# Kernel tuning notes

Measured on AMD Instinct MI355X. Metric: run time of the kernel, lower is better.

The kernel has to match this reference:

```python
import jax, jax.numpy as jnp
import numpy as np

N = 32768        # num_nodes
D = 256          # hidden_dim
H = 8            # num_heads
DH = D // H      # head_dim
S = 4            # num_scales
CS = max(3, N // 10)          # cluster size (pos=None path)
C = (N + CS - 1) // CS        # num_clusters
EPS = 1e-5


def setup_inputs() -> dict:
    key = jax.random.key(0)
    ks = jax.random.split(key, 16)
    w = 0.02
    return {
        "x": jax.random.normal(ks[0], (N, D), dtype=jnp.float32),
        "edge_index": jax.random.randint(ks[1], (2, 16 * N), 0, N),
        "batch": jnp.zeros((N,), dtype=jnp.int32),
        # per-scale AttentionPooling params (stacked over S)
        "Wk": jax.random.normal(ks[2], (S, D, D), dtype=jnp.float32) * w,
        "bk": jnp.zeros((S, D), dtype=jnp.float32),
        "Wv": jax.random.normal(ks[3], (S, D, D), dtype=jnp.float32) * w,
        "bv": jnp.zeros((S, D), dtype=jnp.float32),
        "Wo": jax.random.normal(ks[4], (S, D, D), dtype=jnp.float32) * w,
        "bo": jnp.zeros((S, D), dtype=jnp.float32),
        "pool_query": jax.random.normal(ks[5], (S, H, DH), dtype=jnp.float32),
        # scale fusion params
        "Wf1": jax.random.normal(ks[6], (S * D, D), dtype=jnp.float32) * w,
        "bf1": jnp.zeros((D,), dtype=jnp.float32),
        "ln_g": jnp.ones((D,), dtype=jnp.float32),
        "ln_b": jnp.zeros((D,), dtype=jnp.float32),
        "Wf2": jax.random.normal(ks[7], (D, D), dtype=jnp.float32) * w,
        "bf2": jnp.zeros((D,), dtype=jnp.float32),
    }


def reference(x, edge_index, batch, Wk, bk, Wv, bv, Wo, bo, pool_query,
              Wf1, bf1, ln_g, ln_b, Wf2, bf2):
    # clusters from pos=None branch: arange(N) // cluster_size (same at all scales)
    clusters = jnp.arange(N) // CS                                  # [N]
    scale = DH ** -0.5

    # all S scales vectorized (params stacked on axis s)
    keys = (jnp.einsum('nd,sde->nse', x, Wk) + bk).reshape(N, S, H, DH)
    values = (jnp.einsum('nd,sde->nse', x, Wv) + bv).reshape(N, S, H, DH)

    # pool_query is identical for every node -> scores[n,s,h] = <k, q> * scale
    scores = jnp.einsum('nshd,shd->nsh', keys, pool_query) * scale  # [N,S,H]

    # per-cluster softmax over the node dim (segment softmax)
    smax = jax.ops.segment_max(scores, clusters, num_segments=C)    # [C,S,H]
    ex = jnp.exp(scores - smax[clusters])
    denom = jax.ops.segment_sum(ex, clusters, num_segments=C)
    weights = ex / denom[clusters]                                  # [N,S,H]

    # attended values, scatter-mean over clusters
    attended = (weights[..., None] * values).reshape(N, S, D)       # [N,S,D]
    counts = jax.ops.segment_sum(jnp.ones((N,), dtype=x.dtype), clusters, num_segments=C)
    pooled = jax.ops.segment_sum(attended, clusters, num_segments=C) / counts[:, None, None]

    # out_proj then gather back to nodes
    out = jnp.einsum('csd,sde->cse', pooled, Wo) + bo               # [C,S,D]
    node = out[clusters]                                            # [N,S,D]

    # scale fusion: Linear -> LayerNorm -> GELU -> (Dropout eval=id) -> Linear
    combined = node.reshape(N, S * D)
    h = combined @ Wf1 + bf1
    mu = jnp.mean(h, axis=-1, keepdims=True)
    var = jnp.mean(jnp.square(h - mu), axis=-1, keepdims=True)
    h = (h - mu) / jnp.sqrt(var + EPS) * ln_g + ln_b
    h = jax.nn.gelu(h, approximate=False)
    fused = h @ Wf2 + bf2                                           # [N,D]
    return fused
```

## Files before the change

kernel.cpp:

```cpp
#include <hip/hip_runtime.h>
#include <math.h>


namespace {
constexpr int N   = 32768;
constexpr int CS  = 3276;
constexpr int CPN = 128;
constexpr int CPC = 26;
constexpr int NB  = CPC*10 + 1;

constexpr size_t CQ_OFF   = 0;
constexpr size_t WQBF_OFF = 32;
constexpr size_t PART_OFF = WQBF_OFF + 4096;
constexpr size_t PS_OFF   = PART_OFF + (size_t)NB*8192;
constexpr size_t XW_OFF   = PS_OFF + 352;
constexpr size_t PL_OFF   = XW_OFF + 90112;
constexpr size_t OL_OFF   = PL_OFF + 11264;
constexpr size_t HP_OFF   = OL_OFF + 11264;
constexpr size_t HL_OFF   = HP_OFF + 11264;
constexpr size_t FP_OFF   = HL_OFF + 2816;
}

typedef __attribute__((ext_vector_type(8))) short short8;
typedef __attribute__((ext_vector_type(4))) float f32x4;

__device__ __forceinline__ unsigned f2bf(float f){
  unsigned u = __float_as_uint(f);
  unsigned r = u + 0x7FFFu + ((u >> 16) & 1u);
  return r >> 16;
}

__global__ __launch_bounds__(256) void ka(const float* __restrict__ Wk, const float* __restrict__ bk,
                                          const float* __restrict__ pq, float* __restrict__ ws){
  int b = blockIdx.x, t = threadIdx.x;
  const float scale = 0.17677669529663688f;
  if (b < 32){
    __shared__ float row[256];
    int s = b >> 3, h = b & 7;
    const float* wrow = Wk + ((size_t)s<<16) + (size_t)t*256 + h*32;
    const float* q = pq + (s*8 + h)*32;
    float a = 0.f;
#pragma unroll
    for (int j=0;j<32;j++) a = fmaf(wrow[j], q[j], a);
    row[t] = a*scale;
    __syncthreads();
    if (t < 32){
      int ks = t & 7, kg2 = t >> 3;
      const float* src = row + ks*32 + kg2*8;
      uint4 p;
      p.x = f2bf(src[0]) | (f2bf(src[1]) << 16);
      p.y = f2bf(src[2]) | (f2bf(src[3]) << 16);
      p.z = f2bf(src[4]) | (f2bf(src[5]) << 16);
      p.w = f2bf(src[6]) | (f2bf(src[7]) << 16);
      int Nt = b >> 4, l15b = b & 15;
      ((uint4*)(ws + WQBF_OFF))[(size_t)(Nt*8 + ks)*64 + l15b + 16*kg2] = p;
    }
  } else {
    if (t < 32){
      int s = t >> 3, h = t & 7;
      const float* br = bk + s*256 + h*32;
      const float* q = pq + t*32;
      float a = 0.f;
#pragma unroll
      for (int j=0;j<32;j++) a = fmaf(br[j], q[j], a);
      ws[CQ_OFF + t] = a*scale;
    }
    for (int i = t; i < 352; i += 256) ws[PS_OFF + i] = 0.f;
  }
}

__global__ __launch_bounds__(512,6) void kbd7(const float* __restrict__ x, float* __restrict__ ws){
  int b = blockIdx.x, t = threadIdx.x;
  int c  = (b < 260) ? (b / CPC) : 10;
  int wi = (b < 260) ? (b % CPC) : 0;
  int n0 = c*CS + wi*CPN;
  int n1 = min(n0 + CPN, min((c+1)*CS, N));
  int cnt = n1 - n0;

  __shared__ unsigned short xtb[64*264];
  __shared__ float sw[64*36];
  __shared__ float psb[16*32];

  int wv = t >> 6, lane = t & 63;
  int Mt = wv & 3, Nt = wv >> 2;
  int l15 = lane & 15, kg = lane >> 4;
  int arow = Mt*16 + l15;
  uint4 bfr[8];
  const uint4* WQBF4 = (const uint4*)(ws + WQBF_OFF);
#pragma unroll
  for (int ks=0; ks<8; ++ks) bfr[ks] = WQBF4[(size_t)(Nt*8 + ks)*64 + lane];
  float cqv = ws[CQ_OFF + Nt*16 + l15];
  int shc = Nt*16 + l15;

  int shq = t >> 6, dq = t & 63;
  float acc[16];
#pragma unroll
  for (int q=0;q<16;q++) acc[q] = 0.f;
  float s4 = 0.f;

  const float4* X4 = (const float4*)x;
  int nst = (cnt + 63) >> 6;
  for (int st=0; st<nst; ++st){
    int base = n0 + st*64;
    int lim = min(64, cnt - st*64);
    if (st) __syncthreads();
#pragma unroll
    for (int k=0;k<8;k++){
      int f = t + k*512;
      int j = f >> 6, c4 = f & 63;
      if (base + j < N){
        float4 v = X4[(size_t)(base+j)*64 + c4];
        uint2 p;
        p.x = f2bf(v.x) | (f2bf(v.y) << 16);
        p.y = f2bf(v.z) | (f2bf(v.w) << 16);
        *(uint2*)(xtb + j*264 + c4*4) = p;
      }
    }
    __syncthreads();
    f32x4 acc1 = {0.f, 0.f, 0.f, 0.f};
#pragma unroll
    for (int ks=0; ks<8; ++ks){
      union { uint4 q; short8 v; } A, B;
      A.q = *(const uint4*)(xtb + arow*264 + ks*32 + kg*8);
      B.q = bfr[ks];
      acc1 = __builtin_amdgcn_mfma_f32_16x16x32_bf16(A.v, B.v, acc1, 0, 0, 0);
    }
#pragma unroll
    for (int r=0;r<4;r++){
      int jl = Mt*16 + kg*4 + r;
      float e = __expf(acc1[r] + cqv);
      sw[jl*36 + shc] = e;
      if (st*64 + jl < cnt) s4 += e;
    }
    __syncthreads();
#pragma unroll 4
    for (int j=0;j<lim;++j){
      uint2 u = *(const uint2*)(xtb + j*264 + dq*4);
      float x0 = __uint_as_float(u.x << 16);
      float x1 = __uint_as_float(u.x & 0xffff0000u);
      float x2 = __uint_as_float(u.y << 16);
      float x3 = __uint_as_float(u.y & 0xffff0000u);
      float4 wv2 = *(const float4*)(sw + j*36 + shq*4);
      acc[0]  = fmaf(wv2.x, x0, acc[0]);  acc[1]  = fmaf(wv2.x, x1, acc[1]);
      acc[2]  = fmaf(wv2.x, x2, acc[2]);  acc[3]  = fmaf(wv2.x, x3, acc[3]);
      acc[4]  = fmaf(wv2.y, x0, acc[4]);  acc[5]  = fmaf(wv2.y, x1, acc[5]);
      acc[6]  = fmaf(wv2.y, x2, acc[6]);  acc[7]  = fmaf(wv2.y, x3, acc[7]);
      acc[8]  = fmaf(wv2.z, x0, acc[8]);  acc[9]  = fmaf(wv2.z, x1, acc[9]);
      acc[10] = fmaf(wv2.z, x2, acc[10]); acc[11] = fmaf(wv2.z, x3, acc[11]);
      acc[12] = fmaf(wv2.w, x0, acc[12]); acc[13] = fmaf(wv2.w, x1, acc[13]);
      acc[14] = fmaf(wv2.w, x2, acc[14]); acc[15] = fmaf(wv2.w, x3, acc[15]);
    }
  }
  psb[(Mt*4 + kg)*32 + shc] = s4;
  __syncthreads();
  if (t < 32){
    float S = 0.f;
#pragma unroll
    for (int k=0;k<16;k++) S += psb[k*32 + t];
    unsafeAtomicAdd(ws + PS_OFF + (size_t)c*32 + t, S);
  }
  float* pr = ws + PART_OFF + (size_t)b*8192;
#pragma unroll
  for (int i=0;i<4;i++)
    *(float4*)(pr + (size_t)(shq*4+i)*256 + dq*4) =
      make_float4(acc[i*4], acc[i*4+1], acc[i*4+2], acc[i*4+3]);
}

__global__ __launch_bounds__(256) void ke2(float* __restrict__ ws){
  int b = blockIdx.x, t = threadIdx.x;
  int c = b >> 5, sh = b & 31;
  int nch = (c < 10) ? CPC : 1;
  int cb  = (c < 10) ? c*CPC : 260;
  float rden = 1.0f / ws[PS_OFF + (size_t)c*32 + sh];
  const float* part = ws + PART_OFF + (size_t)sh*256 + t;
  float a = 0.f;
  for (int k=0;k<nch;k++) a += part[(size_t)(cb+k)*8192];
  ws[XW_OFF + (size_t)c*8192 + (size_t)sh*256 + t] = a * rden;
}

__global__ __launch_bounds__(256) void kp(float* __restrict__ ws,
    const float* __restrict__ Wv, const float* __restrict__ bv){
  int b = blockIdx.x; int c = b >> 4, rem = b & 15, s = rem >> 2, eq = rem & 3;
  int t = threadIdx.x, e64 = t & 63, dq = t >> 6;
  int e = eq*64 + e64, h = e >> 5;
  const float* xr = ws + XW_OFF + (size_t)c*8192 + (size_t)(s*8 + h)*256 + dq*64;
  const float* wv = Wv + (size_t)s*65536 + (size_t)(dq*64)*256 + e;
  float a = 0.f;
#pragma unroll 8
  for (int d=0; d<64; ++d) a = fmaf(wv[(size_t)d*256], xr[d], a);
  __shared__ float red[4][64];
  red[dq][e64] = a;
  __syncthreads();
  if (t < 64){
    float rcnt = (c < 10) ? (1.0f/(float)CS) : 0.125f;
    float p = (red[0][t]+red[1][t]+red[2][t]+red[3][t] + bv[s*256 + eq*64 + t]) * rcnt;
    ws[PL_OFF + (size_t)c*1024 + s*256 + eq*64 + t] = p;
  }
}

__global__ __launch_bounds__(256) void ko(float* __restrict__ ws,
    const float* __restrict__ Wo, const float* __restrict__ bo){
  int b = blockIdx.x; int c = b >> 4, rem = b & 15, s = rem >> 2, eq = rem & 3;
  int t = threadIdx.x, e64 = t & 63, dq = t >> 6;
  int e = eq*64 + e64;
  const float* pr = ws + PL_OFF + (size_t)c*1024 + s*256 + dq*64;
  const float* wo = Wo + (size_t)s*65536 + (size_t)(dq*64)*256 + e;
  float a = 0.f;
#pragma unroll 8
  for (int d=0; d<64; ++d) a = fmaf(wo[(size_t)d*256], pr[d], a);
  __shared__ float red[4][64];
  red[dq][e64] = a;
  __syncthreads();
  if (t < 64)
    ws[OL_OFF + (size_t)c*1024 + s*256 + eq*64 + t] =
      red[0][t]+red[1][t]+red[2][t]+red[3][t] + bo[s*256 + eq*64 + t];
}

__global__ __launch_bounds__(256) void kf1(const float* __restrict__ Wf1, float* __restrict__ ws){
  int b = blockIdx.x; int c = b >> 4, fq = (b >> 2) & 3, kq = b & 3;
  int t = threadIdx.x, f64 = t & 63, ks = t >> 6;
  const float* ol = ws + OL_OFF + (size_t)c*1024 + kq*256 + ks*64;
  const float* wf = Wf1 + (size_t)(kq*256 + ks*64)*256 + fq*64 + f64;
  float a = 0.f;
#pragma unroll 8
  for (int i=0; i<64; ++i) a = fmaf(wf[(size_t)i*256], ol[i], a);
  __shared__ float red[4][64];
  red[ks][f64] = a;
  __syncthreads();
  if (t < 64)
    ws[HP_OFF + (size_t)(c*4 + kq)*256 + fq*64 + t] = red[0][t]+red[1][t]+red[2][t]+red[3][t];
}

__global__ __launch_bounds__(256) void kln(float* __restrict__ ws, const float* __restrict__ bf1,
    const float* __restrict__ lng, const float* __restrict__ lnb){
  int c = blockIdx.x, t = threadIdx.x;
  __shared__ float rs1[4], rs2[4];
  float hacc = bf1[t];
#pragma unroll
  for (int q=0;q<4;q++) hacc += ws[HP_OFF + (size_t)(c*4+q)*256 + t];
  float s1 = hacc, s2v = hacc*hacc;
  for (int off=32; off>0; off>>=1){ s1 += __shfl_down(s1, off, 64); s2v += __shfl_down(s2v, off, 64); }
  int wid = t>>6, lane = t&63;
  if (lane==0){ rs1[wid]=s1; rs2[wid]=s2v; }
  __syncthreads();
  float S1 = rs1[0]+rs1[1]+rs1[2]+rs1[3];
  float S2 = rs2[0]+rs2[1]+rs2[2]+rs2[3];
  float mu = S1*(1.0f/256.0f);
  float var = S2*(1.0f/256.0f) - mu*mu;
  float rsig = rsqrtf(var + 1e-5f);
  float hn = (hacc - mu)*rsig*lng[t] + lnb[t];
  float ge = 0.5f*hn*(1.0f + erff(hn*0.70710678118654752f));
  ws[HL_OFF + (size_t)c*256 + t] = ge;
}

__global__ __launch_bounds__(256) void kf2(const float* __restrict__ Wf2, float* __restrict__ ws){
  int b = blockIdx.x; int c = b >> 4, gq = (b >> 2) & 3, kq = b & 3;
  int t = threadIdx.x, g64 = t & 63, ks = t >> 6;
  const float* hp = ws + HL_OFF + (size_t)c*256 + kq*64 + ks*16;
  const float* wf = Wf2 + (size_t)(kq*64 + ks*16)*256 + gq*64 + g64;
  float a = 0.f;
#pragma unroll
  for (int i=0; i<16; ++i) a = fmaf(wf[(size_t)i*256], hp[i], a);
  __shared__ float red[4][64];
  red[ks][g64] = a;
  __syncthreads();
  if (t < 64)
    ws[FP_OFF + (size_t)(c*4 + kq)*256 + gq*64 + t] = red[0][t]+red[1][t]+red[2][t]+red[3][t];
}

__global__ __launch_bounds__(256) void kbc2(const float* __restrict__ ws, float4* __restrict__ out,
                                            const float* __restrict__ bf2){
  unsigned bidx = blockIdx.x, t = threadIdx.x;
  unsigned idx = bidx*256u + t;
  unsigned c = (bidx*4u) / (unsigned)CS;
  __shared__ float4 row[64];
  if (t < 64){
    const float4* FP4 = (const float4*)(ws + FP_OFF);
    float4 s0 = FP4[(c*4+0)*64 + t];
    float4 s1 = FP4[(c*4+1)*64 + t];
    float4 s2 = FP4[(c*4+2)*64 + t];
    float4 s3 = FP4[(c*4+3)*64 + t];
    float4 bb = ((const float4*)bf2)[t];
    row[t] = make_float4(s0.x+s1.x+s2.x+s3.x+bb.x, s0.y+s1.y+s2.y+s3.y+bb.y,
                         s0.z+s1.z+s2.z+s3.z+bb.z, s0.w+s1.w+s2.w+s3.w+bb.w);
  }
  __syncthreads();
  out[idx] = row[t & 63u];
}

extern "C" void kernel_launch(void* const* d_in, const int* in_sizes, int n_in,
                              void* d_out, int out_size, void* d_ws, size_t ws_size,
                              hipStream_t stream) {
  const float* x   = (const float*)d_in[0];
  const float* Wk  = (const float*)d_in[3];
  const float* bk  = (const float*)d_in[4];
  const float* Wv  = (const float*)d_in[5];
  const float* bv  = (const float*)d_in[6];
  const float* Wo  = (const float*)d_in[7];
  const float* bo  = (const float*)d_in[8];
  const float* pq  = (const float*)d_in[9];
  const float* Wf1 = (const float*)d_in[10];
  const float* bf1 = (const float*)d_in[11];
  const float* lng = (const float*)d_in[12];
  const float* lnb = (const float*)d_in[13];
  const float* Wf2 = (const float*)d_in[14];
  const float* bf2 = (const float*)d_in[15];
  float* ws = (float*)d_ws;
  float4* out = (float4*)d_out;

  hipLaunchKernelGGL(ka,   dim3(33),   dim3(256), 0, stream, Wk, bk, pq, ws);
  hipLaunchKernelGGL(kbd7, dim3(NB),   dim3(512), 0, stream, x, ws);
  hipLaunchKernelGGL(ke2,  dim3(352),  dim3(256), 0, stream, ws);
  hipLaunchKernelGGL(kp,   dim3(176),  dim3(256), 0, stream, ws, Wv, bv);
  hipLaunchKernelGGL(ko,   dim3(176),  dim3(256), 0, stream, ws, Wo, bo);
  hipLaunchKernelGGL(kf1,  dim3(176),  dim3(256), 0, stream, Wf1, ws);
  hipLaunchKernelGGL(kln,  dim3(11),   dim3(256), 0, stream, ws, bf1, lng, lnb);
  hipLaunchKernelGGL(kf2,  dim3(176),  dim3(256), 0, stream, Wf2, ws);
  hipLaunchKernelGGL(kbc2, dim3(8192), dim3(256), 0, stream, ws, out, bf2);
}
```

Before: 70.44 us.

## Drop LDS staging of x in pooling kernel, halve chunk size, fuse LayerNorm into Wf2

The pooling kernel no longer stages bf16-converted x tiles in shared memory. Each wave now loads its MFMA A-operand straight from global memory, and the weighted-value accumulation reads fp32 x directly from global memory. Each block now handles 64 nodes instead of 128, which doubles the block count to 521 and lowers the occupancy hint. The LayerNorm+GELU kernel is merged into the Wf2 matvec kernel, which recomputes the normalization per block and saves one launch. The pooled sum now uses full-precision x instead of bf16 x, and x is read twice from global memory/cache rather than once.

```diff
diff --git a/kernel.cpp b/kernel.cpp
--- a/kernel.cpp
+++ b/kernel.cpp
@@ -5,8 +5,7 @@
 namespace {
 constexpr int N   = 32768;
 constexpr int CS  = 3276;
-constexpr int CPN = 128;
-constexpr int CPC = 26;
+constexpr int CPC = 52;
 constexpr int NB  = CPC*10 + 1;
 
 constexpr size_t CQ_OFF   = 0;
@@ -17,8 +16,7 @@
 constexpr size_t PL_OFF   = XW_OFF + 90112;
 constexpr size_t OL_OFF   = PL_OFF + 11264;
 constexpr size_t HP_OFF   = OL_OFF + 11264;
-constexpr size_t HL_OFF   = HP_OFF + 11264;
-constexpr size_t FP_OFF   = HL_OFF + 2816;
+constexpr size_t FP_OFF   = HP_OFF + 11264;
 }
 
 typedef __attribute__((ext_vector_type(8))) short short8;
@@ -69,89 +67,49 @@
   }
 }
 
-__global__ __launch_bounds__(512,6) void kbd7(const float* __restrict__ x, float* __restrict__ ws){
+__global__ __launch_bounds__(512,4) void kbd8(const float* __restrict__ x, float* __restrict__ ws){
   int b = blockIdx.x, t = threadIdx.x;
-  int c  = (b < 260) ? (b / CPC) : 10;
-  int wi = (b < 260) ? (b % CPC) : 0;
-  int n0 = c*CS + wi*CPN;
-  int n1 = min(n0 + CPN, min((c+1)*CS, N));
+  int c  = (b < 520) ? (b / CPC) : 10;
+  int wi = (b < 520) ? (b % CPC) : 0;
+  int n0 = c*CS + wi*64;
+  int n1 = min(n0 + 64, min((c+1)*CS, N));
   int cnt = n1 - n0;
 
-  __shared__ unsigned short xtb[64*264];
   __shared__ float sw[64*36];
   __shared__ float psb[16*32];
 
   int wv = t >> 6, lane = t & 63;
-  int Mt = wv & 3, Nt = wv >> 2;
-  int l15 = lane & 15, kg = lane >> 4;
-  int arow = Mt*16 + l15;
-  uint4 bfr[8];
-  const uint4* WQBF4 = (const uint4*)(ws + WQBF_OFF);
-#pragma unroll
-  for (int ks=0; ks<8; ++ks) bfr[ks] = WQBF4[(size_t)(Nt*8 + ks)*64 + lane];
-  float cqv = ws[CQ_OFF + Nt*16 + l15];
-  int shc = Nt*16 + l15;
-
-  int shq = t >> 6, dq = t & 63;
-  float acc[16];
-#pragma unroll
-  for (int q=0;q<16;q++) acc[q] = 0.f;
-  float s4 = 0.f;
-
-  const float4* X4 = (const float4*)x;
-  int nst = (cnt + 63) >> 6;
-  for (int st=0; st<nst; ++st){
-    int base = n0 + st*64;
-    int lim = min(64, cnt - st*64);
-    if (st) __syncthreads();
-#pragma unroll
-    for (int k=0;k<8;k++){
-      int f = t + k*512;
-      int j = f >> 6, c4 = f & 63;
-      if (base + j < N){
-        float4 v = X4[(size_t)(base+j)*64 + c4];
-        uint2 p;
-        p.x = f2bf(v.x) | (f2bf(v.y) << 16);
-        p.y = f2bf(v.z) | (f2bf(v.w) << 16);
-        *(uint2*)(xtb + j*264 + c4*4) = p;
-      }
-    }
-    __syncthreads();
+  {
+    int Mt = wv & 3, Nt = wv >> 2;
+    int l15 = lane & 15, kg = lane >> 4;
+    int grow = min(n0 + Mt*16 + l15, N-1);
+    const float* xrow = x + (size_t)grow*256;
+    const uint4* WQBF4 = (const uint4*)(ws + WQBF_OFF);
+    float cqv = ws[CQ_OFF + Nt*16 + l15];
     f32x4 acc1 = {0.f, 0.f, 0.f, 0.f};
 #pragma unroll
     for (int ks=0; ks<8; ++ks){
+      float4 x0 = *(const float4*)(xrow + ks*32 + kg*8);
+      float4 x1 = *(const float4*)(xrow + ks*32 + kg*8 + 4);
       union { uint4 q; short8 v; } A, B;
-      A.q = *(const uint4*)(xtb + arow*264 + ks*32 + kg*8);
-      B.q = bfr[ks];
+      A.q.x = f2bf(x0.x) | (f2bf(x0.y) << 16);
+      A.q.y = f2bf(x0.z) | (f2bf(x0.w) << 16);
+      A.q.z = f2bf(x1.x) | (f2bf(x1.y) << 16);
+      A.q.w = f2bf(x1.z) | (f2bf(x1.w) << 16);
+      B.q = WQBF4[(size_t)(Nt*8 + ks)*64 + lane];
       acc1 = __builtin_amdgcn_mfma_f32_16x16x32_bf16(A.v, B.v, acc1, 0, 0, 0);
     }
+    int shc = Nt*16 + l15;
+    float s4 = 0.f;
 #pragma unroll
     for (int r=0;r<4;r++){
       int jl = Mt*16 + kg*4 + r;
       float e = __expf(acc1[r] + cqv);
       sw[jl*36 + shc] = e;
-      if (st*64 + jl < cnt) s4 += e;
-    }
-    __syncthreads();
-#pragma unroll 4
-    for (int j=0;j<lim;++j){
-      uint2 u = *(const uint2*)(xtb + j*264 + dq*4);
-      float x0 = __uint_as_float(u.x << 16);
-      float x1 = __uint_as_float(u.x & 0xffff0000u);
-      float x2 = __uint_as_float(u.y << 16);
-      float x3 = __uint_as_float(u.y & 0xffff0000u);
-      float4 wv2 = *(const float4*)(sw + j*36 + shq*4);
-      acc[0]  = fmaf(wv2.x, x0, acc[0]);  acc[1]  = fmaf(wv2.x, x1, acc[1]);
-      acc[2]  = fmaf(wv2.x, x2, acc[2]);  acc[3]  = fmaf(wv2.x, x3, acc[3]);
-      acc[4]  = fmaf(wv2.y, x0, acc[4]);  acc[5]  = fmaf(wv2.y, x1, acc[5]);
-      acc[6]  = fmaf(wv2.y, x2, acc[6]);  acc[7]  = fmaf(wv2.y, x3, acc[7]);
-      acc[8]  = fmaf(wv2.z, x0, acc[8]);  acc[9]  = fmaf(wv2.z, x1, acc[9]);
-      acc[10] = fmaf(wv2.z, x2, acc[10]); acc[11] = fmaf(wv2.z, x3, acc[11]);
-      acc[12] = fmaf(wv2.w, x0, acc[12]); acc[13] = fmaf(wv2.w, x1, acc[13]);
-      acc[14] = fmaf(wv2.w, x2, acc[14]); acc[15] = fmaf(wv2.w, x3, acc[15]);
-    }
-  }
-  psb[(Mt*4 + kg)*32 + shc] = s4;
+      if (jl < cnt) s4 += e;
+    }
+    psb[(Mt*4 + kg)*32 + shc] = s4;
+  }
   __syncthreads();
   if (t < 32){
     float S = 0.f;
@@ -159,10 +117,30 @@
     for (int k=0;k<16;k++) S += psb[k*32 + t];
     unsafeAtomicAdd(ws + PS_OFF + (size_t)c*32 + t, S);
   }
+
+  int dqin = lane & 7, shq = lane >> 3;
+  int dbase = wv*32 + dqin*4;
+  const float* xp = x + (size_t)n0*256 + dbase;
+  float acc[16];
+#pragma unroll
+  for (int q=0;q<16;q++) acc[q] = 0.f;
+#pragma unroll 8
+  for (int j=0;j<cnt;++j){
+    float4 xv = *(const float4*)(xp + (size_t)j*256);
+    float4 wv2 = *(const float4*)(sw + j*36 + shq*4);
+    acc[0]  = fmaf(wv2.x, xv.x, acc[0]);  acc[1]  = fmaf(wv2.x, xv.y, acc[1]);
+    acc[2]  = fmaf(wv2.x, xv.z, acc[2]);  acc[3]  = fmaf(wv2.x, xv.w, acc[3]);
+    acc[4]  = fmaf(wv2.y, xv.x, acc[4]);  acc[5]  = fmaf(wv2.y, xv.y, acc[5]);
+    acc[6]  = fmaf(wv2.y, xv.z, acc[6]);  acc[7]  = fmaf(wv2.y, xv.w, acc[7]);
+    acc[8]  = fmaf(wv2.z, xv.x, acc[8]);  acc[9]  = fmaf(wv2.z, xv.y, acc[9]);
+    acc[10] = fmaf(wv2.z, xv.z, acc[10]); acc[11] = fmaf(wv2.z, xv.w, acc[11]);
+    acc[12] = fmaf(wv2.w, xv.x, acc[12]); acc[13] = fmaf(wv2.w, xv.y, acc[13]);
+    acc[14] = fmaf(wv2.w, xv.z, acc[14]); acc[15] = fmaf(wv2.w, xv.w, acc[15]);
+  }
   float* pr = ws + PART_OFF + (size_t)b*8192;
 #pragma unroll
   for (int i=0;i<4;i++)
-    *(float4*)(pr + (size_t)(shq*4+i)*256 + dq*4) =
+    *(float4*)(pr + (size_t)(shq*4+i)*256 + dbase) =
       make_float4(acc[i*4], acc[i*4+1], acc[i*4+2], acc[i*4+3]);
 }
 
@@ -170,7 +148,7 @@
   int b = blockIdx.x, t = threadIdx.x;
   int c = b >> 5, sh = b & 31;
   int nch = (c < 10) ? CPC : 1;
-  int cb  = (c < 10) ? c*CPC : 260;
+  int cb  = (c < 10) ? c*CPC : 520;
   float rden = 1.0f / ws[PS_OFF + (size_t)c*32 + sh];
   const float* part = ws + PART_OFF + (size_t)sh*256 + t;
   float a = 0.f;
@@ -231,9 +209,11 @@
     ws[HP_OFF + (size_t)(c*4 + kq)*256 + fq*64 + t] = red[0][t]+red[1][t]+red[2][t]+red[3][t];
 }
 
-__global__ __launch_bounds__(256) void kln(float* __restrict__ ws, const float* __restrict__ bf1,
-    const float* __restrict__ lng, const float* __restrict__ lnb){
-  int c = blockIdx.x, t = threadIdx.x;
+__global__ __launch_bounds__(256) void kf2b(const float* __restrict__ Wf2, float* __restrict__ ws,
+    const float* __restrict__ bf1, const float* __restrict__ lng, const float* __restrict__ lnb){
+  int b = blockIdx.x; int c = b >> 4, gq = (b >> 2) & 3, kq = b & 3;
+  int t = threadIdx.x;
+  __shared__ float hl[256];
   __shared__ float rs1[4], rs2[4];
   float hacc = bf1[t];
 #pragma unroll
@@ -249,18 +229,14 @@
   float var = S2*(1.0f/256.0f) - mu*mu;
   float rsig = rsqrtf(var + 1e-5f);
   float hn = (hacc - mu)*rsig*lng[t] + lnb[t];
-  float ge = 0.5f*hn*(1.0f + erff(hn*0.70710678118654752f));
-  ws[HL_OFF + (size_t)c*256 + t] = ge;
-}
-
-__global__ __launch_bounds__(256) void kf2(const float* __restrict__ Wf2, float* __restrict__ ws){
-  int b = blockIdx.x; int c = b >> 4, gq = (b >> 2) & 3, kq = b & 3;
-  int t = threadIdx.x, g64 = t & 63, ks = t >> 6;
-  const float* hp = ws + HL_OFF + (size_t)c*256 + kq*64 + ks*16;
+  hl[t] = 0.5f*hn*(1.0f + erff(hn*0.70710678118654752f));
+  __syncthreads();
+  int g64 = t & 63, ks = t >> 6;
+  const float* hh = hl + kq*64 + ks*16;
   const float* wf = Wf2 + (size_t)(kq*64 + ks*16)*256 + gq*64 + g64;
   float a = 0.f;
 #pragma unroll
-  for (int i=0; i<16; ++i) a = fmaf(wf[(size_t)i*256], hp[i], a);
+  for (int i=0; i<16; ++i) a = fmaf(wf[(size_t)i*256], hh[i], a);
   __shared__ float red[4][64];
   red[ks][g64] = a;
   __syncthreads();
@@ -309,12 +285,11 @@
   float4* out = (float4*)d_out;
 
   hipLaunchKernelGGL(ka,   dim3(33),   dim3(256), 0, stream, Wk, bk, pq, ws);
-  hipLaunchKernelGGL(kbd7, dim3(NB),   dim3(512), 0, stream, x, ws);
+  hipLaunchKernelGGL(kbd8, dim3(NB),   dim3(512), 0, stream, x, ws);
   hipLaunchKernelGGL(ke2,  dim3(352),  dim3(256), 0, stream, ws);
   hipLaunchKernelGGL(kp,   dim3(176),  dim3(256), 0, stream, ws, Wv, bv);
   hipLaunchKernelGGL(ko,   dim3(176),  dim3(256), 0, stream, ws, Wo, bo);
   hipLaunchKernelGGL(kf1,  dim3(176),  dim3(256), 0, stream, Wf1, ws);
-  hipLaunchKernelGGL(kln,  dim3(11),   dim3(256), 0, stream, ws, bf1, lng, lnb);
-  hipLaunchKernelGGL(kf2,  dim3(176),  dim3(256), 0, stream, Wf2, ws);
+  hipLaunchKernelGGL(kf2b, dim3(176),  dim3(256), 0, stream, Wf2, ws, bf1, lng, lnb);
   hipLaunchKernelGGL(kbc2, dim3(8192), dim3(256), 0, stream, ws, out, bf2);
 }
```

Result: slower. 77.47 us (+10.0%).

## Split pooling kernel into 64-node blocks and fuse LayerNorm-GELU into second fusion GEMV

Applied to the files above, without the earlier changes.

The attention-pooling kernel now gives each block one 64-node chunk instead of looping over 128 nodes in two stages. This doubles the block count to 520+1 and drops the per-stage loop and its barriers, with occupancy hints lowered from 6 to 4. The price is twice as many partial buffers for ke2 to reduce. The separate LayerNorm+GELU kernel is folded into the Wf2 GEMV kernel, which removes one launch and one workspace round-trip but recomputes the LayerNorm redundantly in each of the 16 blocks per cluster.

```diff
diff --git a/kernel.cpp b/kernel.cpp
--- a/kernel.cpp
+++ b/kernel.cpp
@@ -5,8 +5,7 @@
 namespace {
 constexpr int N   = 32768;
 constexpr int CS  = 3276;
-constexpr int CPN = 128;
-constexpr int CPC = 26;
+constexpr int CPC = 52;
 constexpr int NB  = CPC*10 + 1;
 
 constexpr size_t CQ_OFF   = 0;
@@ -17,8 +16,7 @@
 constexpr size_t PL_OFF   = XW_OFF + 90112;
 constexpr size_t OL_OFF   = PL_OFF + 11264;
 constexpr size_t HP_OFF   = OL_OFF + 11264;
-constexpr size_t HL_OFF   = HP_OFF + 11264;
-constexpr size_t FP_OFF   = HL_OFF + 2816;
+constexpr size_t FP_OFF   = HP_OFF + 11264;
 }
 
 typedef __attribute__((ext_vector_type(8))) short short8;
@@ -69,12 +67,12 @@
   }
 }
 
-__global__ __launch_bounds__(512,6) void kbd7(const float* __restrict__ x, float* __restrict__ ws){
+__global__ __launch_bounds__(512,4) void kbd9(const float* __restrict__ x, float* __restrict__ ws){
   int b = blockIdx.x, t = threadIdx.x;
-  int c  = (b < 260) ? (b / CPC) : 10;
-  int wi = (b < 260) ? (b % CPC) : 0;
-  int n0 = c*CS + wi*CPN;
-  int n1 = min(n0 + CPN, min((c+1)*CS, N));
+  int c  = (b < 520) ? (b / CPC) : 10;
+  int wi = (b < 520) ? (b % CPC) : 0;
+  int n0 = c*CS + wi*64;
+  int n1 = min(n0 + 64, min((c+1)*CS, N));
   int cnt = n1 - n0;
 
   __shared__ unsigned short xtb[64*264];
@@ -92,72 +90,66 @@
   float cqv = ws[CQ_OFF + Nt*16 + l15];
   int shc = Nt*16 + l15;
 
+  const float4* X4 = (const float4*)x;
+#pragma unroll
+  for (int k=0;k<8;k++){
+    int f = t + k*512;
+    int j = f >> 6, c4 = f & 63;
+    if (n0 + j < N){
+      float4 v = X4[(size_t)(n0+j)*64 + c4];
+      uint2 p;
+      p.x = f2bf(v.x) | (f2bf(v.y) << 16);
+      p.y = f2bf(v.z) | (f2bf(v.w) << 16);
+      *(uint2*)(xtb + j*264 + c4*4) = p;
+    }
+  }
+  __syncthreads();
+
+  f32x4 acc1 = {0.f, 0.f, 0.f, 0.f};
+#pragma unroll
+  for (int ks=0; ks<8; ++ks){
+    union { uint4 q; short8 v; } A, B;
+    A.q = *(const uint4*)(xtb + arow*264 + ks*32 + kg*8);
+    B.q = bfr[ks];
+    acc1 = __builtin_amdgcn_mfma_f32_16x16x32_bf16(A.v, B.v, acc1, 0, 0, 0);
+  }
+  float s4 = 0.f;
+#pragma unroll
+  for (int r=0;r<4;r++){
+    int jl = Mt*16 + kg*4 + r;
+    float e = __expf(acc1[r] + cqv);
+    sw[jl*36 + shc] = e;
+    if (jl < cnt) s4 += e;
+  }
+  psb[(Mt*4 + kg)*32 + shc] = s4;
+  __syncthreads();
+  if (t < 32){
+    float S = 0.f;
+#pragma unroll
+    for (int k=0;k<16;k++) S += psb[k*32 + t];
+    unsafeAtomicAdd(ws + PS_OFF + (size_t)c*32 + t, S);
+  }
+
   int shq = t >> 6, dq = t & 63;
   float acc[16];
 #pragma unroll
   for (int q=0;q<16;q++) acc[q] = 0.f;
-  float s4 = 0.f;
-
-  const float4* X4 = (const float4*)x;
-  int nst = (cnt + 63) >> 6;
-  for (int st=0; st<nst; ++st){
-    int base = n0 + st*64;
-    int lim = min(64, cnt - st*64);
-    if (st) __syncthreads();
-#pragma unroll
-    for (int k=0;k<8;k++){
-      int f = t + k*512;
-      int j = f >> 6, c4 = f & 63;
-      if (base + j < N){
-        float4 v = X4[(size_t)(base+j)*64 + c4];
-        uint2 p;
-        p.x = f2bf(v.x) | (f2bf(v.y) << 16);
-        p.y = f2bf(v.z) | (f2bf(v.w) << 16);
-        *(uint2*)(xtb + j*264 + c4*4) = p;
-      }
-    }
-    __syncthreads();
-    f32x4 acc1 = {0.f, 0.f, 0.f, 0.f};
-#pragma unroll
-    for (int ks=0; ks<8; ++ks){
-      union { uint4 q; short8 v; } A, B;
-      A.q = *(const uint4*)(xtb + arow*264 + ks*32 + kg*8);
-      B.q = bfr[ks];
-      acc1 = __builtin_amdgcn_mfma_f32_16x16x32_bf16(A.v, B.v, acc1, 0, 0, 0);
-    }
-#pragma unroll
-    for (int r=0;r<4;r++){
-      int jl = Mt*16 + kg*4 + r;
-      float e = __expf(acc1[r] + cqv);
-      sw[jl*36 + shc] = e;
-      if (st*64 + jl < cnt) s4 += e;
-    }
-    __syncthreads();
 #pragma unroll 4
-    for (int j=0;j<lim;++j){
-      uint2 u = *(const uint2*)(xtb + j*264 + dq*4);
-      float x0 = __uint_as_float(u.x << 16);
-      float x1 = __uint_as_float(u.x & 0xffff0000u);
-      float x2 = __uint_as_float(u.y << 16);
-      float x3 = __uint_as_float(u.y & 0xffff0000u);
-      float4 wv2 = *(const float4*)(sw + j*36 + shq*4);
-      acc[0]  = fmaf(wv2.x, x0, acc[0]);  acc[1]  = fmaf(wv2.x, x1, acc[1]);
-      acc[2]  = fmaf(wv2.x, x2, acc[2]);  acc[3]  = fmaf(wv2.x, x3, acc[3]);
-      acc[4]  = fmaf(wv2.y, x0, acc[4]);  acc[5]  = fmaf(wv2.y, x1, acc[5]);
-      acc[6]  = fmaf(wv2.y, x2, acc[6]);  acc[7]  = fmaf(wv2.y, x3, acc[7]);
-      acc[8]  = fmaf(wv2.z, x0, acc[8]);  acc[9]  = fmaf(wv2.z, x1, acc[9]);
-      acc[10] = fmaf(wv2.z, x2, acc[10]); acc[11] = fmaf(wv2.z, x3, acc[11]);
-      acc[12] = fmaf(wv2.w, x0, acc[12]); acc[13] = fmaf(wv2.w, x1, acc[13]);
-      acc[14] = fmaf(wv2.w, x2, acc[14]); acc[15] = fmaf(wv2.w, x3, acc[15]);
-    }
-  }
-  psb[(Mt*4 + kg)*32 + shc] = s4;
-  __syncthreads();
-  if (t < 32){
-    float S = 0.f;
-#pragma unroll
-    for (int k=0;k<16;k++) S += psb[k*32 + t];
-    unsafeAtomicAdd(ws + PS_OFF + (size_t)c*32 + t, S);
+  for (int j=0;j<cnt;++j){
+    uint2 u = *(const uint2*)(xtb + j*264 + dq*4);
+    float x0 = __uint_as_float(u.x << 16);
+    float x1 = __uint_as_float(u.x & 0xffff0000u);
+    float x2 = __uint_as_float(u.y << 16);
+    float x3 = __uint_as_float(u.y & 0xffff0000u);
+    float4 wv2 = *(const float4*)(sw + j*36 + shq*4);
+    acc[0]  = fmaf(wv2.x, x0, acc[0]);  acc[1]  = fmaf(wv2.x, x1, acc[1]);
+    acc[2]  = fmaf(wv2.x, x2, acc[2]);  acc[3]  = fmaf(wv2.x, x3, acc[3]);
+    acc[4]  = fmaf(wv2.y, x0, acc[4]);  acc[5]  = fmaf(wv2.y, x1, acc[5]);
+    acc[6]  = fmaf(wv2.y, x2, acc[6]);  acc[7]  = fmaf(wv2.y, x3, acc[7]);
+    acc[8]  = fmaf(wv2.z, x0, acc[8]);  acc[9]  = fmaf(wv2.z, x1, acc[9]);
+    acc[10] = fmaf(wv2.z, x2, acc[10]); acc[11] = fmaf(wv2.z, x3, acc[11]);
+    acc[12] = fmaf(wv2.w, x0, acc[12]); acc[13] = fmaf(wv2.w, x1, acc[13]);
+    acc[14] = fmaf(wv2.w, x2, acc[14]); acc[15] = fmaf(wv2.w, x3, acc[15]);
   }
   float* pr = ws + PART_OFF + (size_t)b*8192;
 #pragma unroll
@@ -170,7 +162,7 @@
   int b = blockIdx.x, t = threadIdx.x;
   int c = b >> 5, sh = b & 31;
   int nch = (c < 10) ? CPC : 1;
-  int cb  = (c < 10) ? c*CPC : 260;
+  int cb  = (c < 10) ? c*CPC : 520;
   float rden = 1.0f / ws[PS_OFF + (size_t)c*32 + sh];
   const float* part = ws + PART_OFF + (size_t)sh*256 + t;
   float a = 0.f;
@@ -231,9 +223,11 @@
     ws[HP_OFF + (size_t)(c*4 + kq)*256 + fq*64 + t] = red[0][t]+red[1][t]+red[2][t]+red[3][t];
 }
 
-__global__ __launch_bounds__(256) void kln(float* __restrict__ ws, const float* __restrict__ bf1,
-    const float* __restrict__ lng, const float* __restrict__ lnb){
-  int c = blockIdx.x, t = threadIdx.x;
+__global__ __launch_bounds__(256) void kf2b(const float* __restrict__ Wf2, float* __restrict__ ws,
+    const float* __restrict__ bf1, const float* __restrict__ lng, const float* __restrict__ lnb){
+  int b = blockIdx.x; int c = b >> 4, gq = (b >> 2) & 3, kq = b & 3;
+  int t = threadIdx.x;
+  __shared__ float hl[256];
   __shared__ float rs1[4], rs2[4];
   float hacc = bf1[t];
 #pragma unroll
@@ -249,18 +243,14 @@
   float var = S2*(1.0f/256.0f) - mu*mu;
   float rsig = rsqrtf(var + 1e-5f);
   float hn = (hacc - mu)*rsig*lng[t] + lnb[t];
-  float ge = 0.5f*hn*(1.0f + erff(hn*0.70710678118654752f));
-  ws[HL_OFF + (size_t)c*256 + t] = ge;
-}
-
-__global__ __launch_bounds__(256) void kf2(const float* __restrict__ Wf2, float* __restrict__ ws){
-  int b = blockIdx.x; int c = b >> 4, gq = (b >> 2) & 3, kq = b & 3;
-  int t = threadIdx.x, g64 = t & 63, ks = t >> 6;
-  const float* hp = ws + HL_OFF + (size_t)c*256 + kq*64 + ks*16;
+  hl[t] = 0.5f*hn*(1.0f + erff(hn*0.70710678118654752f));
+  __syncthreads();
+  int g64 = t & 63, ks = t >> 6;
+  const float* hh = hl + kq*64 + ks*16;
   const float* wf = Wf2 + (size_t)(kq*64 + ks*16)*256 + gq*64 + g64;
   float a = 0.f;
 #pragma unroll
-  for (int i=0; i<16; ++i) a = fmaf(wf[(size_t)i*256], hp[i], a);
+  for (int i=0; i<16; ++i) a = fmaf(wf[(size_t)i*256], hh[i], a);
   __shared__ float red[4][64];
   red[ks][g64] = a;
   __syncthreads();
@@ -309,12 +299,11 @@
   float4* out = (float4*)d_out;
 
   hipLaunchKernelGGL(ka,   dim3(33),   dim3(256), 0, stream, Wk, bk, pq, ws);
-  hipLaunchKernelGGL(kbd7, dim3(NB),   dim3(512), 0, stream, x, ws);
+  hipLaunchKernelGGL(kbd9, dim3(NB),   dim3(512), 0, stream, x, ws);
   hipLaunchKernelGGL(ke2,  dim3(352),  dim3(256), 0, stream, ws);
   hipLaunchKernelGGL(kp,   dim3(176),  dim3(256), 0, stream, ws, Wv, bv);
   hipLaunchKernelGGL(ko,   dim3(176),  dim3(256), 0, stream, ws, Wo, bo);
   hipLaunchKernelGGL(kf1,  dim3(176),  dim3(256), 0, stream, Wf1, ws);
-  hipLaunchKernelGGL(kln,  dim3(11),   dim3(256), 0, stream, ws, bf1, lng, lnb);
-  hipLaunchKernelGGL(kf2,  dim3(176),  dim3(256), 0, stream, Wf2, ws);
+  hipLaunchKernelGGL(kf2b, dim3(176),  dim3(256), 0, stream, Wf2, ws, bf1, lng, lnb);
   hipLaunchKernelGGL(kbc2, dim3(8192), dim3(256), 0, stream, ws, out, bf2);
 }
```

Result: no change. 69.43 us (-1.4%).
